# Kernel optimization log

Measured on AMD Instinct MI355X. Metric: run time of the kernel, lower is better.

The kernel has to match this reference:

```python
import jax, jax.numpy as jnp
import numpy as np

B, D_IN, H = 16384, 512, 1024


def setup_inputs() -> dict:
    key = jax.random.key(0)
    ks = jax.random.split(key, 12)
    s_in = 1.0 / np.sqrt(D_IN)
    s_h = 1.0 / np.sqrt(H)
    d = {
        "input_x": jax.random.normal(ks[0], (B, D_IN), jnp.float32),
        "h_old": jax.random.normal(ks[1], (B, H), jnp.float32),
        "c_old": jax.random.normal(ks[2], (B, H), jnp.float32),
    }
    names_U = ["Ui", "Uf", "Uo", "Uc"]
    names_W = ["Wi", "Wf", "Wo", "Wc"]
    for i, n in enumerate(names_U):
        d[n + "_w"] = jax.random.normal(ks[3 + i], (D_IN, H), jnp.float32) * s_in
        d[n + "_b"] = jnp.zeros((H,), jnp.float32)
    for i, n in enumerate(names_W):
        d[n + "_w"] = jax.random.normal(ks[7 + i], (H, H), jnp.float32) * s_h
        d[n + "_b"] = jnp.zeros((H,), jnp.float32)
    return d


def reference(input_x, h_old, c_old,
              Ui_w, Ui_b, Wi_w, Wi_b,
              Uf_w, Uf_b, Wf_w, Wf_b,
              Uo_w, Uo_b, Wo_w, Wo_b,
              Uc_w, Uc_b, Wc_w, Wc_b):
    # Fuse the 8 small GEMMs into 2: concatenate gate projections along the
    # output dim (math identical to 8 separate Dense layers + adds).
    U = jnp.concatenate([Ui_w, Uf_w, Uo_w, Uc_w], axis=1)   # [D_in, 4H]
    W = jnp.concatenate([Wi_w, Wf_w, Wo_w, Wc_w], axis=1)   # [H, 4H]
    b = jnp.concatenate([Ui_b + Wi_b, Uf_b + Wf_b, Uo_b + Wo_b, Uc_b + Wc_b])
    gates = input_x @ U + h_old @ W + b                      # [B, 4H]
    i_t, f_t, o_t, g_t = jnp.split(gates, 4, axis=1)
    i_t = jax.nn.sigmoid(i_t)
    f_t = jax.nn.sigmoid(f_t)
    o_t = jax.nn.sigmoid(o_t)
    c_t = jnp.tanh(g_t)
    c = i_t * c_t + f_t * c_old
    h_new = o_t * jnp.tanh(c)
    return (h_new, c)
```

## Files before the change

kernel.cpp:

```cpp
#include <hip/hip_runtime.h>
#include <hip/hip_bf16.h>
#include <stdint.h>

#define B_ROWS 16384
#define D_IN   512
#define H_DIM  1024
#define K_TOT  1536
#define NT     24
#define NIT    12

typedef __attribute__((ext_vector_type(8)))  short bf16x8;
typedef __attribute__((ext_vector_type(16))) float f32x16;
typedef __attribute__((ext_vector_type(4)))  float float4v;
typedef __attribute__((ext_vector_type(8)))  unsigned short u16x8;

__device__ __forceinline__ unsigned short f2bf(float f) {
    uint32_t u = __float_as_uint(f);
    u = (u + 0x7FFFu + ((u >> 16) & 1u)) >> 16;
    return (unsigned short)u;
}

__global__ void cvt_A(const float* __restrict__ x, const float* __restrict__ h,
                      unsigned short* __restrict__ A) {
    int t   = blockIdx.x * blockDim.x + threadIdx.x;
    int row = t / 192;
    int seg = t % 192;
    const float* src;
    if (seg < 64) src = x + (size_t)row * D_IN + seg * 8;
    else          src = h + (size_t)row * H_DIM + (seg - 64) * 8;
    float4v v0 = *(const float4v*)(src);
    float4v v1 = *(const float4v*)(src + 4);
    u16x8 o;
    o[0] = f2bf(v0[0]); o[1] = f2bf(v0[1]); o[2] = f2bf(v0[2]); o[3] = f2bf(v0[3]);
    o[4] = f2bf(v1[0]); o[5] = f2bf(v1[1]); o[6] = f2bf(v1[2]); o[7] = f2bf(v1[3]);
    *(u16x8*)(A + (size_t)row * K_TOT + seg * 8) = o;
}

__global__ void cvt_B(const float* __restrict__ Ui, const float* __restrict__ Uf,
                      const float* __restrict__ Uo, const float* __restrict__ Uc,
                      const float* __restrict__ Wi, const float* __restrict__ Wf,
                      const float* __restrict__ Wo, const float* __restrict__ Wc,
                      unsigned short* __restrict__ Bg) {
    int t  = blockIdx.x * blockDim.x + threadIdx.x;
    int c  = t / 192;
    int k8 = t % 192;
    int g  = (c >> 6) & 3;
    int h  = ((c >> 8) << 6) | (c & 63);
    const float* up = (g == 0) ? Ui : (g == 1) ? Uf : (g == 2) ? Uo : Uc;
    const float* wp = (g == 0) ? Wi : (g == 1) ? Wf : (g == 2) ? Wo : Wc;
    int k = k8 * 8;
    u16x8 o;
    if (k < 512) {
        const float* s = up + (size_t)k * H_DIM + h;
        #pragma unroll
        for (int i = 0; i < 8; ++i) o[i] = f2bf(s[(size_t)i * H_DIM]);
    } else {
        const float* s = wp + (size_t)(k - 512) * H_DIM + h;
        #pragma unroll
        for (int i = 0; i < 8; ++i) o[i] = f2bf(s[(size_t)i * H_DIM]);
    }
    *(u16x8*)(Bg + (size_t)c * K_TOT + k) = o;
}

__global__ void cvt_bias(const float* __restrict__ Uib, const float* __restrict__ Ufb,
                         const float* __restrict__ Uob, const float* __restrict__ Ucb,
                         const float* __restrict__ Wib, const float* __restrict__ Wfb,
                         const float* __restrict__ Wob, const float* __restrict__ Wcb,
                         float* __restrict__ bias) {
    int t = blockIdx.x * blockDim.x + threadIdx.x;
    int g = t >> 10, h = t & 1023;
    const float* ub = (g == 0) ? Uib : (g == 1) ? Ufb : (g == 2) ? Uob : Ucb;
    const float* wb = (g == 0) ? Wib : (g == 1) ? Wfb : (g == 2) ? Wob : Wcb;
    bias[t] = ub[h] + wb[h];
}

__global__ __launch_bounds__(512, 2) void lstm_gemm(
        const unsigned short* __restrict__ Ag, const unsigned short* __restrict__ Bg,
        const float* __restrict__ bias, const float* __restrict__ c_old,
        float* __restrict__ out) {
    __shared__ __align__(1024) char lds[131072];

    const int tid = threadIdx.x;
    const int l   = tid & 63;
    const int wv  = tid >> 6;
    const int wm  = wv >> 1;
    const int wn  = wv & 1;

    const int orig = blockIdx.x;
    const int xcd  = orig & 7;
    const int jj   = orig >> 3;
    const int bn   = (xcd & 3) * 4 + (jj & 3);
    const int bm   = (xcd >> 2) * 32 + (jj >> 2);

    const int kg  = (l & 7) ^ (l >> 3);
    const int pr0 = wv * 16 + (l >> 3);
    const int pr1 = pr0 + 8;
    const unsigned short* aP0 = Ag + (size_t)(bm * 256 + pr0) * K_TOT + kg * 8;
    const unsigned short* aP1 = Ag + (size_t)(bm * 256 + pr1) * K_TOT + kg * 8;
    const int cB0 = ((pr0 >> 5) & 1) * 64 + ((pr0 >> 6) & 1) * 32 + (pr0 & 31);
    const int cB1 = ((pr1 >> 5) & 1) * 64 + ((pr1 >> 6) & 1) * 32 + (pr1 & 31);
    const unsigned short* bP0 = Bg + (size_t)(bn * 256 + cB0) * K_TOT + kg * 8;
    const unsigned short* bP1 = Bg + (size_t)(bn * 256 + cB1) * K_TOT + kg * 8;

    const int r31 = l & 31;
    const int h5  = l >> 5;
    int aoffs[2][4], boffs[4][4];
    #pragma unroll
    for (int mm = 0; mm < 2; ++mm) {
        int pr = wm * 64 + mm * 32 + r31;
        #pragma unroll
        for (int ks = 0; ks < 4; ++ks)
            aoffs[mm][ks] = pr * 128 + (((ks * 2 + h5) ^ (pr & 7)) << 4);
    }
    #pragma unroll
    for (int nn = 0; nn < 4; ++nn) {
        int pr = (nn >> 1) * 128 + wn * 64 + (nn & 1) * 32 + r31;
        #pragma unroll
        for (int ks = 0; ks < 4; ++ks)
            boffs[nn][ks] = pr * 128 + (((ks * 2 + h5) ^ (pr & 7)) << 4);
    }

#define STAGE2(TILE, HF, BUF) do {                                                  \
    size_t _so = (size_t)((HF) * 128) * K_TOT + (TILE) * 64;                        \
    char* _da = (char*)lds + (BUF) * 65536 + (HF) * 16384 + wv * 2048;              \
    char* _db = _da + 32768;                                                        \
    __builtin_amdgcn_global_load_lds(                                               \
        (const __attribute__((address_space(1))) void*)(aP0 + _so),                 \
        (__attribute__((address_space(3))) void*)_da, 16, 0, 0);                    \
    __builtin_amdgcn_global_load_lds(                                               \
        (const __attribute__((address_space(1))) void*)(aP1 + _so),                 \
        (__attribute__((address_space(3))) void*)(_da + 1024), 16, 0, 0);           \
    __builtin_amdgcn_global_load_lds(                                               \
        (const __attribute__((address_space(1))) void*)(bP0 + _so),                 \
        (__attribute__((address_space(3))) void*)_db, 16, 0, 0);                    \
    __builtin_amdgcn_global_load_lds(                                               \
        (const __attribute__((address_space(1))) void*)(bP1 + _so),                 \
        (__attribute__((address_space(3))) void*)(_db + 1024), 16, 0, 0);           \
} while (0)

    f32x16 acc[2][4] = {};
    bf16x8 aF[2][4];

#define PH0(BUF, STILE, SBUF) do {                                                  \
    const char* _Ab = (const char*)lds + (BUF) * 65536;                             \
    const char* _Bb = _Ab + 32768;                                                  \
    _Pragma("unroll") for (int mm = 0; mm < 2; ++mm)                                \
        _Pragma("unroll") for (int ks = 0; ks < 4; ++ks)                            \
            aF[mm][ks] = *(const bf16x8*)(_Ab + aoffs[mm][ks]);                     \
    bf16x8 _b[2][4];                                                                \
    _Pragma("unroll") for (int nn = 0; nn < 2; ++nn)                                \
        _Pragma("unroll") for (int ks = 0; ks < 4; ++ks)                            \
            _b[nn][ks] = *(const bf16x8*)(_Bb + boffs[nn][ks]);                     \
    STAGE2(STILE, 1, SBUF);                                                         \
    __builtin_amdgcn_s_setprio(1);                                                  \
    _Pragma("unroll") for (int ks = 0; ks < 4; ++ks)                                \
        _Pragma("unroll") for (int mm = 0; mm < 2; ++mm)                            \
            _Pragma("unroll") for (int nn = 0; nn < 2; ++nn)                        \
                acc[mm][nn] = __builtin_amdgcn_mfma_f32_32x32x16_bf16(              \
                    aF[mm][ks], _b[nn][ks], acc[mm][nn], 0, 0, 0);                  \
    __builtin_amdgcn_s_setprio(0);                                                  \
    asm volatile("s_waitcnt vmcnt(8)\ns_barrier" ::: "memory");                     \
} while (0)

#define PH1(BUF, STILE, SBUF) do {                                                  \
    const char* _Bb = (const char*)lds + (BUF) * 65536 + 32768;                     \
    bf16x8 _b[2][4];                                                                \
    _Pragma("unroll") for (int nn = 0; nn < 2; ++nn)                                \
        _Pragma("unroll") for (int ks = 0; ks < 4; ++ks)                            \
            _b[nn][ks] = *(const bf16x8*)(_Bb + boffs[nn + 2][ks]);                 \
    STAGE2(STILE, 0, SBUF);                                                         \
    __builtin_amdgcn_s_setprio(1);                                                  \
    _Pragma("unroll") for (int ks = 0; ks < 4; ++ks)                                \
        _Pragma("unroll") for (int mm = 0; mm < 2; ++mm)                            \
            _Pragma("unroll") for (int nn = 0; nn < 2; ++nn)                        \
                acc[mm][nn + 2] = __builtin_amdgcn_mfma_f32_32x32x16_bf16(          \
                    aF[mm][ks], _b[nn][ks], acc[mm][nn + 2], 0, 0, 0);              \
    __builtin_amdgcn_s_setprio(0);                                                  \
    asm volatile("s_waitcnt vmcnt(6)\ns_barrier" ::: "memory");                     \
} while (0)

    STAGE2(0, 0, 0);
    STAGE2(0, 1, 0);
    STAGE2(1, 0, 1);
    asm volatile("s_waitcnt vmcnt(6)\ns_barrier" ::: "memory");

    #pragma unroll 1
    for (int i = 0; i < NIT; ++i) {
        const int t1 = 2 * i + 1;
        int t2 = 2 * i + 2; if (t2 >= NT) t2 -= NT;
        int t3 = 2 * i + 3; if (t3 >= NT) t3 -= NT;
        PH0(0, t1, 1);
        PH1(0, t2, 0);
        PH0(1, t2, 0);
        PH1(1, t3, 1);
    }

    const int hh  = bn * 64 + wn * 32 + r31;
    const float bi  = bias[hh];
    const float bff = bias[1024 + hh];
    const float bo  = bias[2048 + hh];
    const float bc  = bias[3072 + hh];

    #pragma unroll
    for (int mm = 0; mm < 2; ++mm) {
        const int rb = bm * 256 + wm * 64 + mm * 32 + 4 * h5;
        #pragma unroll
        for (int r = 0; r < 16; ++r) {
            const int row = rb + (r & 3) + 8 * (r >> 2);
            float iv = acc[mm][0][r] + bi;
            float fv = acc[mm][1][r] + bff;
            float ov = acc[mm][2][r] + bo;
            float gv = acc[mm][3][r] + bc;
            float it = 1.f / (1.f + __expf(-iv));
            float ft = 1.f / (1.f + __expf(-fv));
            float ot = 1.f / (1.f + __expf(-ov));
            float gt = 1.f - 2.f / (1.f + __expf(2.f * gv));
            float co = c_old[(size_t)row * H_DIM + hh];
            float cn = it * gt + ft * co;
            float th = 1.f - 2.f / (1.f + __expf(2.f * cn));
            out[(size_t)row * H_DIM + hh] = ot * th;
            out[(size_t)B_ROWS * H_DIM + (size_t)row * H_DIM + hh] = cn;
        }
    }
#undef PH0
#undef PH1
#undef STAGE2
}

extern "C" void kernel_launch(void* const* d_in, const int* in_sizes, int n_in,
                              void* d_out, int out_size, void* d_ws, size_t ws_size,
                              hipStream_t stream) {
    const float* x  = (const float*)d_in[0];
    const float* h0 = (const float*)d_in[1];
    const float* c0 = (const float*)d_in[2];
    const float* Uw[4] = {(const float*)d_in[3],  (const float*)d_in[5],
                          (const float*)d_in[7],  (const float*)d_in[9]};
    const float* Ub[4] = {(const float*)d_in[4],  (const float*)d_in[6],
                          (const float*)d_in[8],  (const float*)d_in[10]};
    const float* Ww[4] = {(const float*)d_in[11], (const float*)d_in[13],
                          (const float*)d_in[15], (const float*)d_in[17]};
    const float* Wb[4] = {(const float*)d_in[12], (const float*)d_in[14],
                          (const float*)d_in[16], (const float*)d_in[18]};

    unsigned short* Ag = (unsigned short*)d_ws;
    unsigned short* Bg = Ag + (size_t)B_ROWS * K_TOT;
    float* bias        = (float*)(Bg + (size_t)4096 * K_TOT);
    float* out         = (float*)d_out;

    cvt_A<<<12288, 256, 0, stream>>>(x, h0, Ag);
    cvt_B<<<3072, 256, 0, stream>>>(Uw[0], Uw[1], Uw[2], Uw[3],
                                    Ww[0], Ww[1], Ww[2], Ww[3], Bg);
    cvt_bias<<<16, 256, 0, stream>>>(Ub[0], Ub[1], Ub[2], Ub[3],
                                     Wb[0], Wb[1], Wb[2], Wb[3], bias);
    lstm_gemm<<<1024, 512, 0, stream>>>(Ag, Bg, bias, c0, out);
}
```

Baseline: 300.5 us.

## Pre-tile A and B into MFMA fragment order and use a four-slot K=32 pipeline

The conversion kernels now write A and B in a tiled, fragment-ordered layout, so each K=32 tile for a 256-row block sits in one contiguous 16KB chunk. The GEMM then loads fragments with simple linear LDS offsets and no XOR swizzle. The main loop changes from a double-buffered K=64 scheme to a four-slot ring of K=32 stages. The gate interleaving moves from 64-column to 32-column groups so each wave's columns line up with the epilogue. The intent is to cut LDS address arithmetic and bank conflicts and to get contiguous global reads. The cost is smaller per-stage MFMA work, more barriers, and possible LDS bank conflicts because the reads are no longer swizzled.

Result: faster. 274.1 us (-8.8%).

```diff
diff --git a/kernel.cpp b/kernel.cpp
--- a/kernel.cpp
+++ b/kernel.cpp
@@ -6,7 +6,7 @@
 #define D_IN   512
 #define H_DIM  1024
 #define K_TOT  1536
-#define NT     24
+#define NKT    48
 #define NIT    12
 
 typedef __attribute__((ext_vector_type(8)))  short bf16x8;
@@ -21,19 +21,23 @@
 }
 
 __global__ void cvt_A(const float* __restrict__ x, const float* __restrict__ h,
-                      unsigned short* __restrict__ A) {
-    int t   = blockIdx.x * blockDim.x + threadIdx.x;
-    int row = t / 192;
-    int seg = t % 192;
-    const float* src;
-    if (seg < 64) src = x + (size_t)row * D_IN + seg * 8;
-    else          src = h + (size_t)row * H_DIM + (seg - 64) * 8;
+                      unsigned short* __restrict__ Ag) {
+    int t     = blockIdx.x * blockDim.x + threadIdx.x;
+    int lane  = t & 63;
+    int chunk = (t >> 6) & 15;
+    int rest  = t >> 10;
+    int tile  = rest % 48;
+    int bm    = rest / 48;
+    int row   = bm * 256 + (chunk >> 1) * 32 + (lane & 31);
+    int k     = tile * 32 + (chunk & 1) * 16 + (lane >> 5) * 8;
+    const float* src = (k < 512) ? (x + (size_t)row * D_IN + k)
+                                 : (h + (size_t)row * H_DIM + (k - 512));
     float4v v0 = *(const float4v*)(src);
     float4v v1 = *(const float4v*)(src + 4);
     u16x8 o;
     o[0] = f2bf(v0[0]); o[1] = f2bf(v0[1]); o[2] = f2bf(v0[2]); o[3] = f2bf(v0[3]);
     o[4] = f2bf(v1[0]); o[5] = f2bf(v1[1]); o[6] = f2bf(v1[2]); o[7] = f2bf(v1[3]);
-    *(u16x8*)(A + (size_t)row * K_TOT + seg * 8) = o;
+    *(u16x8*)(Ag + (size_t)t * 8) = o;
 }
 
 __global__ void cvt_B(const float* __restrict__ Ui, const float* __restrict__ Uf,
@@ -41,25 +45,29 @@
                       const float* __restrict__ Wi, const float* __restrict__ Wf,
                       const float* __restrict__ Wo, const float* __restrict__ Wc,
                       unsigned short* __restrict__ Bg) {
-    int t  = blockIdx.x * blockDim.x + threadIdx.x;
-    int c  = t / 192;
-    int k8 = t % 192;
-    int g  = (c >> 6) & 3;
-    int h  = ((c >> 8) << 6) | (c & 63);
+    int t     = blockIdx.x * blockDim.x + threadIdx.x;
+    int lane  = t & 63;
+    int chunk = (t >> 6) & 15;
+    int rest  = t >> 10;
+    int tile  = rest % 48;
+    int bn    = rest / 48;
+    int c     = bn * 256 + (chunk >> 1) * 32 + (lane & 31);
+    int g     = (c >> 5) & 3;
+    int hcol  = ((c >> 7) << 5) | (c & 31);
+    int k     = tile * 32 + (chunk & 1) * 16 + (lane >> 5) * 8;
     const float* up = (g == 0) ? Ui : (g == 1) ? Uf : (g == 2) ? Uo : Uc;
     const float* wp = (g == 0) ? Wi : (g == 1) ? Wf : (g == 2) ? Wo : Wc;
-    int k = k8 * 8;
     u16x8 o;
     if (k < 512) {
-        const float* s = up + (size_t)k * H_DIM + h;
+        const float* s = up + (size_t)k * H_DIM + hcol;
         #pragma unroll
         for (int i = 0; i < 8; ++i) o[i] = f2bf(s[(size_t)i * H_DIM]);
     } else {
-        const float* s = wp + (size_t)(k - 512) * H_DIM + h;
+        const float* s = wp + (size_t)(k - 512) * H_DIM + hcol;
         #pragma unroll
         for (int i = 0; i < 8; ++i) o[i] = f2bf(s[(size_t)i * H_DIM]);
     }
-    *(u16x8*)(Bg + (size_t)c * K_TOT + k) = o;
+    *(u16x8*)(Bg + (size_t)t * 8) = o;
 }
 
 __global__ void cvt_bias(const float* __restrict__ Uib, const float* __restrict__ Ufb,
@@ -92,110 +100,67 @@
     const int bn   = (xcd & 3) * 4 + (jj & 3);
     const int bm   = (xcd >> 2) * 32 + (jj >> 2);
 
-    const int kg  = (l & 7) ^ (l >> 3);
-    const int pr0 = wv * 16 + (l >> 3);
-    const int pr1 = pr0 + 8;
-    const unsigned short* aP0 = Ag + (size_t)(bm * 256 + pr0) * K_TOT + kg * 8;
-    const unsigned short* aP1 = Ag + (size_t)(bm * 256 + pr1) * K_TOT + kg * 8;
-    const int cB0 = ((pr0 >> 5) & 1) * 64 + ((pr0 >> 6) & 1) * 32 + (pr0 & 31);
-    const int cB1 = ((pr1 >> 5) & 1) * 64 + ((pr1 >> 6) & 1) * 32 + (pr1 & 31);
-    const unsigned short* bP0 = Bg + (size_t)(bn * 256 + cB0) * K_TOT + kg * 8;
-    const unsigned short* bP1 = Bg + (size_t)(bn * 256 + cB1) * K_TOT + kg * 8;
-
-    const int r31 = l & 31;
-    const int h5  = l >> 5;
-    int aoffs[2][4], boffs[4][4];
-    #pragma unroll
-    for (int mm = 0; mm < 2; ++mm) {
-        int pr = wm * 64 + mm * 32 + r31;
-        #pragma unroll
-        for (int ks = 0; ks < 4; ++ks)
-            aoffs[mm][ks] = pr * 128 + (((ks * 2 + h5) ^ (pr & 7)) << 4);
-    }
-    #pragma unroll
-    for (int nn = 0; nn < 4; ++nn) {
-        int pr = (nn >> 1) * 128 + wn * 64 + (nn & 1) * 32 + r31;
-        #pragma unroll
-        for (int ks = 0; ks < 4; ++ks)
-            boffs[nn][ks] = pr * 128 + (((ks * 2 + h5) ^ (pr & 7)) << 4);
-    }
-
-#define STAGE2(TILE, HF, BUF) do {                                                  \
-    size_t _so = (size_t)((HF) * 128) * K_TOT + (TILE) * 64;                        \
-    char* _da = (char*)lds + (BUF) * 65536 + (HF) * 16384 + wv * 2048;              \
-    char* _db = _da + 32768;                                                        \
-    __builtin_amdgcn_global_load_lds(                                               \
-        (const __attribute__((address_space(1))) void*)(aP0 + _so),                 \
-        (__attribute__((address_space(3))) void*)_da, 16, 0, 0);                    \
-    __builtin_amdgcn_global_load_lds(                                               \
-        (const __attribute__((address_space(1))) void*)(aP1 + _so),                 \
-        (__attribute__((address_space(3))) void*)(_da + 1024), 16, 0, 0);           \
-    __builtin_amdgcn_global_load_lds(                                               \
-        (const __attribute__((address_space(1))) void*)(bP0 + _so),                 \
-        (__attribute__((address_space(3))) void*)_db, 16, 0, 0);                    \
-    __builtin_amdgcn_global_load_lds(                                               \
-        (const __attribute__((address_space(1))) void*)(bP1 + _so),                 \
-        (__attribute__((address_space(3))) void*)(_db + 1024), 16, 0, 0);           \
+    const unsigned short* aT = Ag + (size_t)(wv * 2) * 512 + l * 8;
+    const unsigned short* bT = Bg + (size_t)(wv * 2) * 512 + l * 8;
+    const size_t aTileBase = (size_t)bm * 48 * 8192;
+    const size_t bTileBase = (size_t)bn * 48 * 8192;
+
+#define GLDS(SRC, DST) __builtin_amdgcn_global_load_lds(                            \
+        (const __attribute__((address_space(1))) void*)(SRC),                       \
+        (__attribute__((address_space(3))) void*)(DST), 16, 0, 0)
+
+#define STAGE(ST, SLOT) do {                                                        \
+    const unsigned short* _a = aT + aTileBase + (size_t)(ST) * 8192;                \
+    const unsigned short* _b = bT + bTileBase + (size_t)(ST) * 8192;                \
+    char* _da = (char*)lds + (SLOT) * 32768 + (wv * 2) * 1024;                      \
+    char* _db = _da + 16384;                                                        \
+    GLDS(_a,       _da);        GLDS(_a + 512, _da + 1024);                         \
+    GLDS(_b,       _db);        GLDS(_b + 512, _db + 1024);                         \
 } while (0)
 
     f32x16 acc[2][4] = {};
-    bf16x8 aF[2][4];
-
-#define PH0(BUF, STILE, SBUF) do {                                                  \
-    const char* _Ab = (const char*)lds + (BUF) * 65536;                             \
-    const char* _Bb = _Ab + 32768;                                                  \
+
+#define PHASE(P, ST) do {                                                           \
+    const char* _Ab = (const char*)lds + (P) * 32768 + wm * 4096 + l * 16;          \
+    const char* _Bb = (const char*)lds + (P) * 32768 + 16384 + wn * 8192 + l * 16;  \
+    bf16x8 aF[2][2], bF[4][2];                                                      \
     _Pragma("unroll") for (int mm = 0; mm < 2; ++mm)                                \
-        _Pragma("unroll") for (int ks = 0; ks < 4; ++ks)                            \
-            aF[mm][ks] = *(const bf16x8*)(_Ab + aoffs[mm][ks]);                     \
-    bf16x8 _b[2][4];                                                                \
-    _Pragma("unroll") for (int nn = 0; nn < 2; ++nn)                                \
-        _Pragma("unroll") for (int ks = 0; ks < 4; ++ks)                            \
-            _b[nn][ks] = *(const bf16x8*)(_Bb + boffs[nn][ks]);                     \
-    STAGE2(STILE, 1, SBUF);                                                         \
+        _Pragma("unroll") for (int ks = 0; ks < 2; ++ks)                            \
+            aF[mm][ks] = *(const bf16x8*)(_Ab + mm * 2048 + ks * 1024);             \
+    _Pragma("unroll") for (int nn = 0; nn < 4; ++nn)                                \
+        _Pragma("unroll") for (int ks = 0; ks < 2; ++ks)                            \
+            bF[nn][ks] = *(const bf16x8*)(_Bb + nn * 2048 + ks * 1024);             \
+    STAGE(ST, ((P) + 3) & 3);                                                       \
     __builtin_amdgcn_s_setprio(1);                                                  \
-    _Pragma("unroll") for (int ks = 0; ks < 4; ++ks)                                \
+    _Pragma("unroll") for (int ks = 0; ks < 2; ++ks)                                \
         _Pragma("unroll") for (int mm = 0; mm < 2; ++mm)                            \
-            _Pragma("unroll") for (int nn = 0; nn < 2; ++nn)                        \
+            _Pragma("unroll") for (int nn = 0; nn < 4; ++nn)                        \
                 acc[mm][nn] = __builtin_amdgcn_mfma_f32_32x32x16_bf16(              \
-                    aF[mm][ks], _b[nn][ks], acc[mm][nn], 0, 0, 0);                  \
+                    aF[mm][ks], bF[nn][ks], acc[mm][nn], 0, 0, 0);                  \
     __builtin_amdgcn_s_setprio(0);                                                  \
     asm volatile("s_waitcnt vmcnt(8)\ns_barrier" ::: "memory");                     \
 } while (0)
 
-#define PH1(BUF, STILE, SBUF) do {                                                  \
-    const char* _Bb = (const char*)lds + (BUF) * 65536 + 32768;                     \
-    bf16x8 _b[2][4];                                                                \
-    _Pragma("unroll") for (int nn = 0; nn < 2; ++nn)                                \
-        _Pragma("unroll") for (int ks = 0; ks < 4; ++ks)                            \
-            _b[nn][ks] = *(const bf16x8*)(_Bb + boffs[nn + 2][ks]);                 \
-    STAGE2(STILE, 0, SBUF);                                                         \
-    __builtin_amdgcn_s_setprio(1);                                                  \
-    _Pragma("unroll") for (int ks = 0; ks < 4; ++ks)                                \
-        _Pragma("unroll") for (int mm = 0; mm < 2; ++mm)                            \
-            _Pragma("unroll") for (int nn = 0; nn < 2; ++nn)                        \
-                acc[mm][nn + 2] = __builtin_amdgcn_mfma_f32_32x32x16_bf16(          \
-                    aF[mm][ks], _b[nn][ks], acc[mm][nn + 2], 0, 0, 0);              \
-    __builtin_amdgcn_s_setprio(0);                                                  \
-    asm volatile("s_waitcnt vmcnt(6)\ns_barrier" ::: "memory");                     \
-} while (0)
-
-    STAGE2(0, 0, 0);
-    STAGE2(0, 1, 0);
-    STAGE2(1, 0, 1);
-    asm volatile("s_waitcnt vmcnt(6)\ns_barrier" ::: "memory");
+    STAGE(0, 0); STAGE(1, 1); STAGE(2, 2);
+    asm volatile("s_waitcnt vmcnt(8)\ns_barrier" ::: "memory");
 
     #pragma unroll 1
     for (int i = 0; i < NIT; ++i) {
-        const int t1 = 2 * i + 1;
-        int t2 = 2 * i + 2; if (t2 >= NT) t2 -= NT;
-        int t3 = 2 * i + 3; if (t3 >= NT) t3 -= NT;
-        PH0(0, t1, 1);
-        PH1(0, t2, 0);
-        PH0(1, t2, 0);
-        PH1(1, t3, 1);
+        const int b4 = i * 4;
+        int s0 = b4 + 3;
+        int s1 = b4 + 4; if (s1 >= NKT) s1 -= NKT;
+        int s2 = b4 + 5; if (s2 >= NKT) s2 -= NKT;
+        int s3 = b4 + 6; if (s3 >= NKT) s3 -= NKT;
+        PHASE(0, s0);
+        PHASE(1, s1);
+        PHASE(2, s2);
+        PHASE(3, s3);
     }
-
-    const int hh  = bn * 64 + wn * 32 + r31;
+    asm volatile("s_waitcnt vmcnt(0)" ::: "memory");
+
+    const int r31 = l & 31;
+    const int h5  = l >> 5;
+    const int hh  = (bn * 2 + wn) * 32 + r31;
     const float bi  = bias[hh];
     const float bff = bias[1024 + hh];
     const float bo  = bias[2048 + hh];
@@ -222,9 +187,9 @@
             out[(size_t)B_ROWS * H_DIM + (size_t)row * H_DIM + hh] = cn;
         }
     }
-#undef PH0
-#undef PH1
-#undef STAGE2
+#undef PHASE
+#undef STAGE
+#undef GLDS
 }
 
 extern "C" void kernel_launch(void* const* d_in, const int* in_sizes, int n_in,
```
